# Optimization experiments

Hardware: AMD Instinct MI355X
Metric: run time of the kernel (lower is better)

Reference implementation:

```python
import jax, jax.numpy as jnp
import numpy as np
import math

DIM = 2048
N_HEADS = 16
HEAD_DIM = 128
BATCH = 2
T = 2048
EPS = 1e-5


def setup_inputs() -> dict:
    key = jax.random.key(0)
    ks = jax.random.split(key, 16)
    s = lambda fan_in: 1.0 / math.sqrt(fan_in)
    d = {}
    d['x'] = jax.random.normal(ks[0], (BATCH, T, DIM), dtype=jnp.float32)
    d['start_pos'] = 0
    # attention projections (weights stored [in, out])
    d['wq'] = jax.random.uniform(ks[1], (DIM, N_HEADS * HEAD_DIM), minval=-s(DIM), maxval=s(DIM))
    d['bq'] = jnp.zeros((N_HEADS * HEAD_DIM,), jnp.float32)
    d['wk'] = jax.random.uniform(ks[2], (DIM, HEAD_DIM), minval=-s(DIM), maxval=s(DIM))
    d['bk'] = jnp.zeros((HEAD_DIM,), jnp.float32)
    d['wv'] = jax.random.uniform(ks[3], (DIM, HEAD_DIM), minval=-s(DIM), maxval=s(DIM))
    d['bv'] = jnp.zeros((HEAD_DIM,), jnp.float32)
    d['wo'] = jax.random.uniform(ks[4], (N_HEADS * HEAD_DIM, DIM), minval=-s(N_HEADS * HEAD_DIM), maxval=s(N_HEADS * HEAD_DIM))
    d['bo'] = jnp.zeros((DIM,), jnp.float32)
    # layernorms
    d['ln1_g'] = jnp.ones((DIM,), jnp.float32)
    d['ln1_b'] = jnp.zeros((DIM,), jnp.float32)
    d['ln2_g'] = jnp.ones((DIM,), jnp.float32)
    d['ln2_b'] = jnp.zeros((DIM,), jnp.float32)
    # MLP (dim -> 4*dim -> dim), dropout p=0 is a no-op
    d['w1'] = jax.random.uniform(ks[5], (DIM, 4 * DIM), minval=-s(DIM), maxval=s(DIM))
    d['b1'] = jnp.zeros((4 * DIM,), jnp.float32)
    d['w2'] = jax.random.uniform(ks[6], (4 * DIM, DIM), minval=-s(4 * DIM), maxval=s(4 * DIM))
    d['b2'] = jnp.zeros((DIM,), jnp.float32)
    return d


def _layernorm(h, g, b):
    mu = jnp.mean(h, axis=-1, keepdims=True)
    var = jnp.mean(jnp.square(h - mu), axis=-1, keepdims=True)
    return (h - mu) * jax.lax.rsqrt(var + EPS) * g + b


def reference(x, start_pos, wq, bq, wk, bk, wv, bv, wo, bo, ln1_g, ln1_b, ln2_g, ln2_b, w1, b1, w2, b2):
    B, Tq, D = x.shape
    hd = wk.shape[1]
    H = wq.shape[1] // hd
    # --- MQA attention on pre-LN input (prefill: no kv cache) ---
    h = _layernorm(x, ln1_g, ln1_b)
    q = (h @ wq + bq).reshape(B, Tq, H, hd)          # [B,T,H,hd]
    k = h @ wk + bk                                   # [B,T,hd] single shared head
    v = h @ wv + bv                                   # [B,T,hd]
    scores = jnp.einsum('bthc,bsc->bhts', q, k) / math.sqrt(hd)
    causal = jnp.where(jnp.tril(jnp.ones((Tq, Tq), dtype=bool)), 0.0, -jnp.inf).astype(scores.dtype)
    attn = jax.nn.softmax(scores + causal, axis=-1)   # [B,H,T,T]
    ctx = jnp.einsum('bhts,bsc->bthc', attn, v).reshape(B, Tq, H * hd)
    out = ctx @ wo + bo
    x = x + out
    # --- GELU MLP (exact erf gelu, torch default) ---
    h2 = _layernorm(x, ln2_g, ln2_b)
    x = x + jax.nn.gelu(h2 @ w1 + b1, approximate=False) @ w2 + b2
    k_cat = k[:, None]                                # [B,1,T,hd]
    v_cat = v[:, None]
    return (x, k_cat, v_cat)
```

## Files before the change

### kernel.cpp

```cpp
#include <hip/hip_runtime.h>
#include <stdint.h>

#define DIMSZ 2048
#define HD 128
#define NH 16
#define BATCH 2
#define SEQ 2048
#define MROWS (BATCH*SEQ)
#define FFDIM (4*DIMSZ)
#define NQKV (DIMSZ + 2*HD)

typedef float f32x4 __attribute__((ext_vector_type(4)));
typedef __bf16 bf16x8 __attribute__((ext_vector_type(8)));
typedef __bf16 bf16x2 __attribute__((ext_vector_type(2)));
typedef _Float16 f16x8 __attribute__((ext_vector_type(8)));
typedef __bf16 bf16_t;
typedef _Float16 f16_t;

__device__ __forceinline__ void async16(const void* g, void* l) {
  __builtin_amdgcn_global_load_lds(
      (const __attribute__((address_space(1))) void*)(uintptr_t)g,
      (__attribute__((address_space(3))) void*)(uint32_t)(uintptr_t)l,
      16, 0, 0);
}

__device__ __forceinline__ float gelu_f(float x) {
  return 0.5f * x * (1.0f + erff(x * 0.70710678118654752f));
}

__device__ __forceinline__ void hard_barrier() {
  asm volatile("" ::: "memory");
  __builtin_amdgcn_s_barrier();
  asm volatile("" ::: "memory");
}

__global__ __launch_bounds__(256)
void k_trall(const float* __restrict__ wq, const float* __restrict__ wk,
             const float* __restrict__ wv, const float* __restrict__ wo,
             const float* __restrict__ w1, const float* __restrict__ w2,
             bf16_t* __restrict__ wqkvT, bf16_t* __restrict__ woT,
             bf16_t* __restrict__ w1T, bf16_t* __restrict__ w2T) {
  int bid = blockIdx.x;
  const float* src; bf16_t* dst; int R, C, t0;
  if (bid < 1024)      { src = wq; dst = wqkvT;                        R = 2048; C = 2048; t0 = bid; }
  else if (bid < 1088) { src = wk; dst = wqkvT + (size_t)2048 * 2048;  R = 2048; C = 128;  t0 = bid - 1024; }
  else if (bid < 1152) { src = wv; dst = wqkvT + (size_t)2176 * 2048;  R = 2048; C = 128;  t0 = bid - 1088; }
  else if (bid < 2176) { src = wo; dst = woT;                          R = 2048; C = 2048; t0 = bid - 1152; }
  else if (bid < 6272) { src = w1; dst = w1T;                          R = 2048; C = 8192; t0 = bid - 2176; }
  else                 { src = w2; dst = w2T;                          R = 8192; C = 2048; t0 = bid - 6272; }
  int tc = C >> 6;
  int c0 = (t0 % tc) * 64, r0 = (t0 / tc) * 64;
  __shared__ float tile[64][65];
  int lc = threadIdx.x & 63, lrow = threadIdx.x >> 6;
#pragma unroll
  for (int i = 0; i < 64; i += 4)
    tile[lrow + i][lc] = src[(size_t)(r0 + lrow + i) * C + c0 + lc];
  __syncthreads();
  int rp = threadIdx.x & 31, wc = threadIdx.x >> 5;
#pragma unroll
  for (int i = 0; i < 64; i += 8) {
    int c = wc + i;
    bf16x2 pk = {(bf16_t)tile[2 * rp][c], (bf16_t)tile[2 * rp + 1][c]};
    *(bf16x2*)(dst + (size_t)(c0 + c) * R + r0 + 2 * rp) = pk;
  }
}

__global__ __launch_bounds__(256)
void k_transpose_v(const bf16_t* __restrict__ v, bf16_t* __restrict__ vt) {
  __shared__ bf16_t tile[32][33];
  int b = blockIdx.z;
  int t0 = blockIdx.x * 32, d0 = blockIdx.y * 32;
  int tx = threadIdx.x & 31, ty = threadIdx.x >> 5;
#pragma unroll
  for (int i = 0; i < 32; i += 8)
    tile[ty + i][tx] = v[((size_t)(b * SEQ + t0 + ty + i)) * HD + d0 + tx];
  __syncthreads();
#pragma unroll
  for (int i = 0; i < 32; i += 8)
    vt[((size_t)(b * HD + d0 + ty + i)) * SEQ + t0 + tx] = tile[tx][ty + i];
}

__global__ __launch_bounds__(256)
void k_layernorm(const float* __restrict__ x, const float* __restrict__ g,
                 const float* __restrict__ bb, bf16_t* __restrict__ out) {
  int row = blockIdx.x;
  const float* xr = x + (size_t)row * DIMSZ;
  int t = threadIdx.x;
  float vals[8];
  float s = 0.f, s2 = 0.f;
#pragma unroll
  for (int i = 0; i < 8; ++i) {
    float v = xr[t + i * 256];
    vals[i] = v; s += v; s2 += v * v;
  }
#pragma unroll
  for (int o = 1; o < 64; o <<= 1) { s += __shfl_xor(s, o); s2 += __shfl_xor(s2, o); }
  __shared__ float red[8];
  if ((t & 63) == 0) { red[t >> 6] = s; red[4 + (t >> 6)] = s2; }
  __syncthreads();
  s = red[0] + red[1] + red[2] + red[3];
  s2 = red[4] + red[5] + red[6] + red[7];
  float mu = s * (1.0f / DIMSZ);
  float rstd = rsqrtf(s2 * (1.0f / DIMSZ) - mu * mu + 1e-5f);
  bf16_t* orow = out + (size_t)row * DIMSZ;
#pragma unroll
  for (int i = 0; i < 8; ++i) {
    int c = t + i * 256;
    orow[c] = (bf16_t)((vals[i] - mu) * rstd * g[c] + bb[c]);
  }
}

template <int FN>
__device__ __forceinline__ void gemm8_loop(
    const bf16_t* __restrict__ A, const bf16_t* __restrict__ BT,
    int ld, int Kloop, int bm, int bn, f32x4 (&acc)[8][FN], bf16_t* sh) {
  constexpr int BH = FN >> 1;
  constexpr int BN = FN * 64;
  const int tid = threadIdx.x;
  const int lane = tid & 63, lr = lane & 15, lg = lane >> 4;
  const int wave = tid >> 6, wm = wave >> 2, wn = wave & 3;
  bf16_t* const Ab0 = sh;
  bf16_t* const Bb0 = sh + 32768;
  const bf16_t* const Ag = A + (size_t)bm * 256 * ld;
  const bf16_t* const Bg = BT + (size_t)bn * BN * ld;

  auto stage = [&](const bf16_t* gbase, bf16_t* lbase, int h, int t) {
#pragma unroll
    for (int j = 0; j < 2; ++j) {
      int flat = (tid + j * 512) * 8;
      int r = flat >> 6, kp = flat & 63;
      int ks = kp ^ ((r & 7) << 3);
      async16(gbase + (size_t)(h * 128 + r) * ld + t * 64 + ks, lbase + flat);
    }
  };
  auto stA = [&](int c, int h, int t) { stage(Ag, Ab0 + (c * 2 + h) * 8192, h, t); };
  auto stB = [&](int c, int h, int t) { stage(Bg, Bb0 + (c * BH + h) * 8192, h, t); };

  const int xsw = (lr & 7) << 3;
  bf16x8 a_[4], b_[FN];
  auto lda4 = [&](int c, int m0, int kk) {
    const bf16_t* base = Ab0 + (c * 2 + wm) * 8192;
#pragma unroll
    for (int i = 0; i < 4; ++i)
      a_[i] = *(const bf16x8*)(base + ((m0 + i) * 16 + lr) * 64 + ((kk + lg * 8) ^ xsw));
  };
  auto ldb4 = [&](int c, int kx) {
#pragma unroll
    for (int nf = 0; nf < FN; ++nf) {
      int row = wn * (FN * 16) + nf * 16 + lr;
      const bf16_t* base =
          Bb0 + (c * BH + (BH == 2 ? (row >> 7) : 0)) * 8192 + (row & 127) * 64;
      b_[nf] = *(const bf16x8*)(base + ((kx * 32 + lg * 8) ^ xsw));
    }
  };

#define VMC_GATE                                                     \
  if (BH == 2) { asm volatile("s_waitcnt vmcnt(8)" ::: "memory"); }  \
  else         { asm volatile("s_waitcnt vmcnt(6)" ::: "memory"); }
#define MFMA_Q(M0)                                                   \
  __builtin_amdgcn_s_setprio(1);                                     \
  _Pragma("unroll")                                                  \
  for (int i_ = 0; i_ < 4; ++i_)                                     \
    _Pragma("unroll")                                                \
    for (int nf = 0; nf < FN; ++nf)                                  \
      acc[(M0) + i_][nf] = __builtin_amdgcn_mfma_f32_16x16x32_bf16(  \
          a_[i_], b_[nf], acc[(M0) + i_][nf], 0, 0, 0);              \
  __builtin_amdgcn_s_setprio(0);

  const int nit = Kloop >> 7;

  stB(0, 0, 0); if (BH == 2) stB(0, 1, 0);
  stA(0, 0, 0); stA(0, 1, 0);
  stB(1, 0, 1); if (BH == 2) stB(1, 1, 1);

  for (int i = 0; i < nit; ++i) {
    const int t2 = 2 * i + 2, t3 = 2 * i + 3;
    const bool g2 = (i < nit - 1);
    stA(1, 0, 2 * i + 1); stA(1, 1, 2 * i + 1);
    VMC_GATE;
    hard_barrier();
    lda4(0, 0, 0); ldb4(0, 0);
    MFMA_Q(0)
    hard_barrier();
    lda4(0, 4, 0);
    MFMA_Q(4)
    hard_barrier();
    lda4(0, 0, 32); ldb4(0, 1);
    MFMA_Q(0)
    hard_barrier();
    if (g2) { stB(0, 0, t2); if (BH == 2) stB(0, 1, t2); }
    lda4(0, 4, 32);
    MFMA_Q(4)
    hard_barrier();
    if (g2) {
      stA(0, 0, t2); stA(0, 1, t2);
      VMC_GATE;
    } else {
      asm volatile("s_waitcnt vmcnt(0)" ::: "memory");
    }
    hard_barrier();
    lda4(1, 0, 0); ldb4(1, 0);
    MFMA_Q(0)
    hard_barrier();
    lda4(1, 4, 0);
    MFMA_Q(4)
    hard_barrier();
    lda4(1, 0, 32); ldb4(1, 1);
    MFMA_Q(0)
    hard_barrier();
    if (g2) { stB(1, 0, t3); if (BH == 2) stB(1, 1, t3); }
    lda4(1, 4, 32);
    MFMA_Q(4)
    hard_barrier();
  }
#undef VMC_GATE
#undef MFMA_Q
}

__global__ __launch_bounds__(512, 1)
void k_oproj(const bf16_t* __restrict__ A, const bf16_t* __restrict__ BT,
             const float* __restrict__ bias, const float* __restrict__ res,
             float* __restrict__ outF) {
  extern __shared__ __align__(16) bf16_t sh8[];
  const int nt = DIMSZ / 128;
  int bm = blockIdx.x / nt, bn = blockIdx.x % nt;
  f32x4 acc[8][2] = {};
  gemm8_loop<2>(A, BT, DIMSZ, DIMSZ, bm, bn, acc, sh8);
  int tid = threadIdx.x, wave = tid >> 6, lane = tid & 63, lr = lane & 15, lg = lane >> 4;
  int wm = wave >> 2, wn = wave & 3;
  float* shF = (float*)sh8;
  int rl0 = wm * 128 + lg * 4;
  int cl0 = wn * 32 + lr;
#pragma unroll
  for (int nf = 0; nf < 2; ++nf) {
    int cl = cl0 + nf * 16;
    float bi = bias[bn * 128 + cl];
#pragma unroll
    for (int mf = 0; mf < 8; ++mf)
#pragma unroll
      for (int j = 0; j < 4; ++j)
        shF[(rl0 + mf * 16 + j) * 128 + cl] = acc[mf][nf][j] + bi;
  }
  hard_barrier();
  const float* rbase = res + (size_t)(bm * 256) * DIMSZ + bn * 128;
  float* gbase = outF + (size_t)(bm * 256) * DIMSZ + bn * 128;
#pragma unroll
  for (int s = 0; s < 16; ++s) {
    int flat = s * 512 + tid;
    int row = flat >> 5, cu = flat & 31;
    f32x4 v = *(const f32x4*)(shF + row * 128 + cu * 4);
    f32x4 r4 = *(const f32x4*)(rbase + (size_t)row * DIMSZ + cu * 4);
    *(f32x4*)(gbase + (size_t)row * DIMSZ + cu * 4) = v + r4;
  }
}

__global__ __launch_bounds__(512, 1)
void k_ffn1(const bf16_t* __restrict__ A, const bf16_t* __restrict__ BT,
            const float* __restrict__ bias, bf16_t* __restrict__ outB) {
  extern __shared__ __align__(16) bf16_t sh8[];
  const int nt = FFDIM / 256;
  int bm = blockIdx.x / nt, bn = blockIdx.x % nt;
  f32x4 acc[8][4] = {};
  gemm8_loop<4>(A, BT, DIMSZ, DIMSZ, bm, bn, acc, sh8);
  int tid = threadIdx.x, wave = tid >> 6, lane = tid & 63, lr = lane & 15, lg = lane >> 4;
  int wm = wave >> 2, wn = wave & 3;
  int rl0 = wm * 128 + lg * 4;
  int cl0 = wn * 64 + lr;
#pragma unroll
  for (int nf = 0; nf < 4; ++nf) {
    int cl = cl0 + nf * 16;
    float bi = bias[bn * 256 + cl];
#pragma unroll
    for (int mf = 0; mf < 8; ++mf)
#pragma unroll
      for (int j = 0; j < 4; ++j)
        sh8[(rl0 + mf * 16 + j) * 256 + cl] = (bf16_t)gelu_f(acc[mf][nf][j] + bi);
  }
  hard_barrier();
  bf16_t* gbase = outB + (size_t)(bm * 256) * FFDIM + bn * 256;
#pragma unroll
  for (int s = 0; s < 16; ++s) {
    int flat = s * 512 + tid;
    int row = flat >> 5, cu = flat & 31;
    f32x4 v = *(const f32x4*)(sh8 + row * 256 + cu * 8);
    *(f32x4*)(gbase + (size_t)row * FFDIM + cu * 8) = v;
  }
}

__global__ __launch_bounds__(512, 1)
void k_ffn2(const bf16_t* __restrict__ A, const bf16_t* __restrict__ BT,
            f16_t* __restrict__ p0, f16_t* __restrict__ p1) {
  extern __shared__ __align__(16) bf16_t sh8[];
  int swz = (blockIdx.x & 7) * 32 + (blockIdx.x >> 3);
  int kh = swz >> 7;
  int tile = swz & 127;
  int bm = tile >> 3, bn = tile & 7;
  f32x4 acc[8][4] = {};
  gemm8_loop<4>(A + kh * (FFDIM / 2), BT + kh * (FFDIM / 2), FFDIM, FFDIM / 2,
                bm, bn, acc, sh8);
  int tid = threadIdx.x, wave = tid >> 6, lane = tid & 63, lr = lane & 15, lg = lane >> 4;
  int wm = wave >> 2, wn = wave & 3;
  f16_t* shH = (f16_t*)sh8;
  int rl0 = wm * 128 + lg * 4;
  int cl0 = wn * 64 + lr;
#pragma unroll
  for (int nf = 0; nf < 4; ++nf) {
    int cl = cl0 + nf * 16;
#pragma unroll
    for (int mf = 0; mf < 8; ++mf)
#pragma unroll
      for (int j = 0; j < 4; ++j)
        shH[(rl0 + mf * 16 + j) * 256 + cl] = (f16_t)acc[mf][nf][j];
  }
  hard_barrier();
  f16_t* gbase = (kh ? p1 : p0) + (size_t)(bm * 256) * DIMSZ + bn * 256;
#pragma unroll
  for (int s = 0; s < 16; ++s) {
    int flat = s * 512 + tid;
    int row = flat >> 5, cu = flat & 31;
    f32x4 v = *(const f32x4*)(shH + row * 256 + cu * 8);
    *(f32x4*)(gbase + (size_t)row * DIMSZ + cu * 8) = v;
  }
}

__global__ __launch_bounds__(256)
void k_ffn2red(const f16_t* __restrict__ p0, const f16_t* __restrict__ p1,
               const float* __restrict__ b2, float* __restrict__ outx) {
  int row = blockIdx.x;
  int c0 = threadIdx.x * 8;
  size_t base = (size_t)row * DIMSZ + c0;
  f16x8 a = *(const f16x8*)(p0 + base);
  f16x8 b = *(const f16x8*)(p1 + base);
  f32x4 o0 = *(const f32x4*)(outx + base);
  f32x4 o1 = *(const f32x4*)(outx + base + 4);
  f32x4 b0 = *(const f32x4*)(b2 + c0);
  f32x4 b1 = *(const f32x4*)(b2 + c0 + 4);
#pragma unroll
  for (int i = 0; i < 4; ++i) {
    o0[i] += (float)a[i] + (float)b[i] + b0[i];
    o1[i] += (float)a[4 + i] + (float)b[4 + i] + b1[i];
  }
  *(f32x4*)(outx + base) = o0;
  *(f32x4*)(outx + base + 4) = o1;
}

__global__ __launch_bounds__(512, 1)
void k_qkv(const bf16_t* __restrict__ A, const bf16_t* __restrict__ BT,
           const float* __restrict__ bq, const float* __restrict__ bk,
           const float* __restrict__ bv,
           bf16_t* __restrict__ qb, float* __restrict__ outk,
           float* __restrict__ outv, bf16_t* __restrict__ kbf,
           bf16_t* __restrict__ vbf) {
  extern __shared__ __align__(16) bf16_t sh8[];
  const int nt = NQKV / 256;
  int bm = blockIdx.x / nt, bn = blockIdx.x % nt;
  f32x4 acc[8][4] = {};
  gemm8_loop<4>(A, BT, DIMSZ, DIMSZ, bm, bn, acc, sh8);
  int tid = threadIdx.x, wave = tid >> 6, lane = tid & 63, lr = lane & 15, lg = lane >> 4;
  int wm = wave >> 2, wn = wave & 3;
  int rl0 = wm * 128 + lg * 4;
  int cl0 = wn * 64 + lr;
#pragma unroll
  for (int nf = 0; nf < 4; ++nf) {
    int cl = cl0 + nf * 16;
    int cg = bn * 256 + cl;
    float bi = (cg < 2048) ? bq[cg] : (cg < 2176 ? bk[cg - 2048] : bv[cg - 2176]);
#pragma unroll
    for (int mf = 0; mf < 8; ++mf)
#pragma unroll
      for (int j = 0; j < 4; ++j) {
        float v = acc[mf][nf][j] + bi;
        sh8[(rl0 + mf * 16 + j) * 256 + cl] = (bf16_t)v;
        if (cg >= 2048) {
          int r = bm * 256 + rl0 + mf * 16 + j;
          if (cg < 2176) outk[(size_t)r * HD + (cg - 2048)] = v;
          else           outv[(size_t)r * HD + (cg - 2176)] = v;
        }
      }
  }
  hard_barrier();
#pragma unroll
  for (int s = 0; s < 16; ++s) {
    int flat = s * 512 + tid;
    int row = flat >> 5, cu = flat & 31;
    f32x4 v = *(const f32x4*)(sh8 + row * 256 + cu * 8);
    int r = bm * 256 + row;
    if (bn < 8) {
      *(f32x4*)(qb + (size_t)r * DIMSZ + bn * 256 + cu * 8) = v;
    } else {
      int ce = cu * 8;
      if (ce < 128) *(f32x4*)(kbf + (size_t)r * HD + ce) = v;
      else          *(f32x4*)(vbf + (size_t)r * HD + (ce - 128)) = v;
    }
  }
}

__global__ __launch_bounds__(256, 2)
void k_attn(const bf16_t* __restrict__ q, const bf16_t* __restrict__ k,
            const bf16_t* __restrict__ vt, bf16_t* __restrict__ ctx) {
  __shared__ __align__(16) bf16_t Ks[2][64 * 128];
  __shared__ __align__(16) bf16_t Vs[2][128 * 64];
  __shared__ bf16_t Pw[4][16][72];
  int pp = blockIdx.x, h = blockIdx.y, b = blockIdx.z;
  int tid = threadIdx.x, wave = tid >> 6, lane = tid & 63, lr = lane & 15, lg = lane >> 4;
  const bf16_t* kb = k + (size_t)b * SEQ * HD;
  const bf16_t* vb = vt + (size_t)b * HD * SEQ;

#define STAGE_TILE(buf, s0_)                                                      \
  {                                                                               \
    _Pragma("unroll")                                                             \
    for (int i = 0; i < 4; ++i) {                                                 \
      int flat = (i * 256 + tid) * 8;                                             \
      int kr = flat >> 7, kc = flat & 127;                                        \
      int ksrc = (((kc >> 3) ^ (kr & 7)) << 3) | (kc & 7);                        \
      async16(kb + (size_t)((s0_) + kr) * HD + ksrc, (void*)(Ks[buf] + flat));    \
      int vr = flat >> 6, vc = flat & 63;                                         \
      int vsrc = (((vc >> 3) ^ (vr & 7)) << 3) | (vc & 7);                        \
      async16(vb + (size_t)vr * SEQ + (s0_) + vsrc, (void*)(Vs[buf] + flat));     \
    }                                                                             \
  }

  for (int half = 0; half < 2; ++half) {
    int qt = half ? (31 - pp) : pp;
    int q0 = qt * 64;
    int qw = q0 + wave * 16;
    const bf16_t* qbase = q + ((size_t)(b * SEQ + qw + lr)) * DIMSZ + h * HD;
    bf16x8 qf[4];
#pragma unroll
    for (int kk = 0; kk < 4; ++kk) qf[kk] = *(const bf16x8*)(qbase + kk * 32 + lg * 8);
    f32x4 o[8] = {};
    float m_[4], l_[4];
#pragma unroll
    for (int j = 0; j < 4; ++j) { m_[j] = -3.0e38f; l_[j] = 0.f; }
    int qglob0 = qw + lg * 4;
    int ntiles = qt + 1;

    STAGE_TILE(0, 0)
    __syncthreads();
    for (int t = 0; t < ntiles; ++t) {
      int cur = t & 1;
      if (t + 1 < ntiles) STAGE_TILE(cur ^ 1, (t + 1) * 64)
      int s0 = t * 64;
      const bf16_t* Kc = Ks[cur];
      const bf16_t* Vc = Vs[cur];
      f32x4 sf[4] = {};
#pragma unroll
      for (int nf = 0; nf < 4; ++nf) {
        int R = nf * 16 + lr;
#pragma unroll
        for (int kk = 0; kk < 4; ++kk)
          sf[nf] = __builtin_amdgcn_mfma_f32_16x16x32_bf16(
              qf[kk],
              *(const bf16x8*)(Kc + R * 128 + (((kk * 4 + lg) ^ (R & 7)) << 3)),
              sf[nf], 0, 0, 0);
      }
#pragma unroll
      for (int nf = 0; nf < 4; ++nf) {
        int col = s0 + nf * 16 + lr;
#pragma unroll
        for (int j = 0; j < 4; ++j) {
          float v = sf[nf][j] * 0.088388347648318447f;
          sf[nf][j] = (col <= qglob0 + j) ? v : -3.0e38f;
        }
      }
      float mx[4];
#pragma unroll
      for (int j = 0; j < 4; ++j)
        mx[j] = fmaxf(fmaxf(sf[0][j], sf[1][j]), fmaxf(sf[2][j], sf[3][j]));
#pragma unroll
      for (int o_ = 1; o_ < 16; o_ <<= 1)
#pragma unroll
        for (int j = 0; j < 4; ++j) mx[j] = fmaxf(mx[j], __shfl_xor(mx[j], o_));
      float fsc[4], mn[4];
#pragma unroll
      for (int j = 0; j < 4; ++j) {
        mn[j] = fmaxf(m_[j], mx[j]);
        fsc[j] = __expf(m_[j] - mn[j]);
        m_[j] = mn[j];
      }
      float ps[4] = {0.f, 0.f, 0.f, 0.f};
#pragma unroll
      for (int nf = 0; nf < 4; ++nf)
#pragma unroll
        for (int j = 0; j < 4; ++j) {
          float pv = __expf(sf[nf][j] - mn[j]);
          ps[j] += pv;
          Pw[wave][lg * 4 + j][nf * 16 + lr] = (bf16_t)pv;
        }
#pragma unroll
      for (int o_ = 1; o_ < 16; o_ <<= 1)
#pragma unroll
        for (int j = 0; j < 4; ++j) ps[j] += __shfl_xor(ps[j], o_);
#pragma unroll
      for (int j = 0; j < 4; ++j) l_[j] = l_[j] * fsc[j] + ps[j];
#pragma unroll
      for (int df = 0; df < 8; ++df)
#pragma unroll
        for (int j = 0; j < 4; ++j) o[df][j] *= fsc[j];
      asm volatile("" ::: "memory");
      bf16x8 pa[2];
#pragma unroll
      for (int kk = 0; kk < 2; ++kk)
        pa[kk] = *(const bf16x8*)(&Pw[wave][lr][kk * 32 + lg * 8]);
#pragma unroll
      for (int df = 0; df < 8; ++df) {
        int R = df * 16 + lr;
#pragma unroll
        for (int kk = 0; kk < 2; ++kk)
          o[df] = __builtin_amdgcn_mfma_f32_16x16x32_bf16(
              pa[kk],
              *(const bf16x8*)(Vc + R * 64 + (((kk * 4 + lg) ^ (R & 7)) << 3)),
              o[df], 0, 0, 0);
      }
      __syncthreads();
    }
    bf16_t* cb = ctx + ((size_t)(b * SEQ + qw)) * DIMSZ + h * HD;
#pragma unroll
    for (int df = 0; df < 8; ++df)
#pragma unroll
      for (int j = 0; j < 4; ++j)
        cb[(size_t)(lg * 4 + j) * DIMSZ + df * 16 + lr] = (bf16_t)(o[df][j] / l_[j]);
  }
#undef STAGE_TILE
}

extern "C" void kernel_launch(void* const* d_in, const int* in_sizes, int n_in,
                              void* d_out, int out_size, void* d_ws, size_t ws_size,
                              hipStream_t stream) {
  const float* x   = (const float*)d_in[0];
  const float* wq  = (const float*)d_in[2];
  const float* bq  = (const float*)d_in[3];
  const float* wk  = (const float*)d_in[4];
  const float* bk  = (const float*)d_in[5];
  const float* wv  = (const float*)d_in[6];
  const float* bv  = (const float*)d_in[7];
  const float* wo  = (const float*)d_in[8];
  const float* bo  = (const float*)d_in[9];
  const float* g1  = (const float*)d_in[10];
  const float* be1 = (const float*)d_in[11];
  const float* g2  = (const float*)d_in[12];
  const float* be2 = (const float*)d_in[13];
  const float* w1  = (const float*)d_in[14];
  const float* bb1 = (const float*)d_in[15];
  const float* w2  = (const float*)d_in[16];
  const float* bb2 = (const float*)d_in[17];

  float* outx = (float*)d_out;
  float* outk = outx + (size_t)MROWS * DIMSZ;
  float* outv = outk + (size_t)MROWS * HD;

  char* p = (char*)d_ws;
  auto alloc = [&](size_t bytes) -> char* {
    char* r = p;
    p += (bytes + 255) & ~(size_t)255;
    return r;
  };
  bf16_t* wqkvT = (bf16_t*)alloc((size_t)NQKV * DIMSZ * 2);
  bf16_t* woT = (bf16_t*)alloc((size_t)DIMSZ * DIMSZ * 2);
  bf16_t* w1T = (bf16_t*)alloc((size_t)FFDIM * DIMSZ * 2);
  bf16_t* w2T = (bf16_t*)alloc((size_t)DIMSZ * FFDIM * 2);
  bf16_t* hb  = (bf16_t*)alloc((size_t)MROWS * DIMSZ * 2);
  bf16_t* qb  = (bf16_t*)alloc((size_t)MROWS * DIMSZ * 2);
  bf16_t* kbf = (bf16_t*)alloc((size_t)MROWS * HD * 2);
  bf16_t* vbf = (bf16_t*)alloc((size_t)MROWS * HD * 2);
  bf16_t* vtb = (bf16_t*)alloc((size_t)BATCH * HD * SEQ * 2);
  bf16_t* f1b = (bf16_t*)alloc((size_t)MROWS * FFDIM * 2);
  f16_t* p0  = (f16_t*)alloc((size_t)MROWS * DIMSZ * 2);
  f16_t* p1  = (f16_t*)alloc((size_t)MROWS * DIMSZ * 2);
  (void)ws_size; (void)in_sizes; (void)n_in; (void)out_size;

  dim3 blk(256);
  const int LDSG = 131072;
  k_trall<<<10368, blk, 0, stream>>>(wq, wk, wv, wo, w1, w2, wqkvT, woT, w1T, w2T);
  k_layernorm<<<MROWS, blk, 0, stream>>>(x, g1, be1, hb);
  k_qkv<<<(MROWS / 256) * (NQKV / 256), 512, LDSG, stream>>>(
      hb, wqkvT, bq, bk, bv, qb, outk, outv, kbf, vbf);
  k_transpose_v<<<dim3(SEQ / 32, HD / 32, BATCH), blk, 0, stream>>>(vbf, vtb);
  k_attn<<<dim3(SEQ / 64 / 2, NH, BATCH), blk, 0, stream>>>(qb, kbf, vtb, hb);
  k_oproj<<<(MROWS / 256) * (DIMSZ / 128), 512, LDSG, stream>>>(hb, woT, bo, x, outx);
  k_layernorm<<<MROWS, blk, 0, stream>>>(outx, g2, be2, qb);
  k_ffn1<<<(MROWS / 256) * (FFDIM / 256), 512, LDSG, stream>>>(qb, w1T, bb1, f1b);
  k_ffn2<<<256, 512, LDSG, stream>>>(f1b, w2T, p0, p1);
  k_ffn2red<<<MROWS, blk, 0, stream>>>(p0, p1, bb2, outx);
}
```

Baseline: 539.9 us.

## Restructure GEMM main loop to load fragments before barrier and issue MFMA after

Reorders the double-buffered GEMM loop so each phase reads its LDS fragments and issues the next async global-to-LDS stage before a barrier plus sched_barrier, then runs the MFMA block. Prefetch depth drops from two stages in flight to one, with a full vmcnt(0) wait once per half-iteration instead of partial waits. The goal is to overlap LDS reads with the previous MFMAs and keep the schedule fixed. The cost is less latency hiding for global loads, which may stall on the vmcnt(0) waits.

Measured after the change: 551.8 us. 1.02x slower.

```diff
diff --git a/kernel.cpp b/kernel.cpp
--- a/kernel.cpp
+++ b/kernel.cpp
@@ -154,9 +154,8 @@
     }
   };
 
-#define VMC_GATE                                                     \
-  if (BH == 2) { asm volatile("s_waitcnt vmcnt(8)" ::: "memory"); }  \
-  else         { asm volatile("s_waitcnt vmcnt(6)" ::: "memory"); }
+#define VMC0 asm volatile("s_waitcnt vmcnt(0)" ::: "memory");
+#define PHASE_SYNC hard_barrier(); __builtin_amdgcn_sched_barrier(0);
 #define MFMA_Q(M0)                                                   \
   __builtin_amdgcn_s_setprio(1);                                     \
   _Pragma("unroll")                                                  \
@@ -169,51 +168,48 @@
 
   const int nit = Kloop >> 7;
 
+  stA(0, 0, 0); stA(0, 1, 0);
   stB(0, 0, 0); if (BH == 2) stB(0, 1, 0);
-  stA(0, 0, 0); stA(0, 1, 0);
-  stB(1, 0, 1); if (BH == 2) stB(1, 1, 1);
+  VMC0;
+  hard_barrier();
 
   for (int i = 0; i < nit; ++i) {
-    const int t2 = 2 * i + 2, t3 = 2 * i + 3;
+    const int t1 = 2 * i + 1, t2 = 2 * i + 2;
     const bool g2 = (i < nit - 1);
-    stA(1, 0, 2 * i + 1); stA(1, 1, 2 * i + 1);
-    VMC_GATE;
-    hard_barrier();
     lda4(0, 0, 0); ldb4(0, 0);
+    PHASE_SYNC
     MFMA_Q(0)
-    hard_barrier();
     lda4(0, 4, 0);
+    stA(1, 0, t1); stA(1, 1, t1);
+    PHASE_SYNC
     MFMA_Q(4)
-    hard_barrier();
     lda4(0, 0, 32); ldb4(0, 1);
+    stB(1, 0, t1); if (BH == 2) stB(1, 1, t1);
+    PHASE_SYNC
     MFMA_Q(0)
-    hard_barrier();
+    lda4(0, 4, 32);
+    VMC0;
+    PHASE_SYNC
+    MFMA_Q(4)
+    lda4(1, 0, 0); ldb4(1, 0);
+    PHASE_SYNC
+    MFMA_Q(0)
+    lda4(1, 4, 0);
+    if (g2) { stA(0, 0, t2); stA(0, 1, t2); }
+    PHASE_SYNC
+    MFMA_Q(4)
+    lda4(1, 0, 32); ldb4(1, 1);
     if (g2) { stB(0, 0, t2); if (BH == 2) stB(0, 1, t2); }
-    lda4(0, 4, 32);
+    PHASE_SYNC
+    MFMA_Q(0)
+    lda4(1, 4, 32);
+    if (g2) { VMC0; }
+    PHASE_SYNC
     MFMA_Q(4)
-    hard_barrier();
-    if (g2) {
-      stA(0, 0, t2); stA(0, 1, t2);
-      VMC_GATE;
-    } else {
-      asm volatile("s_waitcnt vmcnt(0)" ::: "memory");
-    }
-    hard_barrier();
-    lda4(1, 0, 0); ldb4(1, 0);
-    MFMA_Q(0)
-    hard_barrier();
-    lda4(1, 4, 0);
-    MFMA_Q(4)
-    hard_barrier();
-    lda4(1, 0, 32); ldb4(1, 1);
-    MFMA_Q(0)
-    hard_barrier();
-    if (g2) { stB(1, 0, t3); if (BH == 2) stB(1, 1, t3); }
-    lda4(1, 4, 32);
-    MFMA_Q(4)
-    hard_barrier();
-  }
-#undef VMC_GATE
+  }
+  hard_barrier();
+#undef VMC0
+#undef PHASE_SYNC
 #undef MFMA_Q
 }
 
```
